# Optimization experiments

Hardware: AMD Instinct MI355X
Metric: run time of the kernel (lower is better)

Reference implementation:

```python
import jax, jax.numpy as jnp
import numpy as np

N_HEADS = 16

def setup_inputs() -> dict:
    key = jax.random.key(0)
    k1, k2, k3 = jax.random.split(key, 3)
    d = 1024
    x = jax.random.normal(k1, (2, 2048, d), dtype=jnp.float32)
    W_in = jax.random.normal(k2, (d, 3 * d), dtype=jnp.float32) * (d ** -0.5)
    W_out = jax.random.normal(k3, (d, d), dtype=jnp.float32) * (d ** -0.5)
    return {"x": x, "W_in": W_in, "W_out": W_out}

def reference(x, W_in, W_out):
    B, S, D = x.shape
    H = N_HEADS
    Dh = D // H
    qkv = x @ W_in                                  # [B,S,3D]
    q, k, v = jnp.split(qkv, 3, axis=-1)
    # [B,S,D] -> [B,H,S,Dh]
    q = q.reshape(B, S, H, Dh).transpose(0, 2, 1, 3)
    k = k.reshape(B, S, H, Dh).transpose(0, 2, 1, 3)
    v = v.reshape(B, S, H, Dh).transpose(0, 2, 1, 3)
    scores = jnp.einsum('bhqd,bhkd->bhqk', q, k)    # [B,H,S,S]
    causal = jnp.triu(jnp.ones((S, S), dtype=bool), k=1)
    scores = jnp.where(causal, -jnp.inf, scores)
    scores = scores / jnp.sqrt(jnp.asarray(Dh, scores.dtype))
    attn = jax.nn.softmax(scores, axis=-1)
    out = jnp.einsum('bhqk,bhkd->bhqd', attn, v)    # [B,H,S,Dh]
    out = out.transpose(0, 2, 1, 3).reshape(B, S, D)
    return out @ W_out
```

## Files before the change

kernel.cpp:

```cpp
#include <hip/hip_runtime.h>
#include <cstdint>
#include <cstddef>

typedef __bf16 bf16;
typedef bf16  bf16x4  __attribute__((ext_vector_type(4)));
typedef bf16  bf16x8  __attribute__((ext_vector_type(8)));
typedef float floatx4 __attribute__((ext_vector_type(4)));

#define BATCH 2
#define SEQ   2048
#define DIM   1024
#define NH    16
#define DH    64
#define D3    3072
#define MROWS 4096

__device__ __forceinline__ void gld16(void* lds, const void* gptr) {
  __builtin_amdgcn_global_load_lds(
      (const __attribute__((address_space(1))) unsigned int*)gptr,
      (__attribute__((address_space(3))) unsigned int*)lds, 16, 0, 0);
}

__global__ __launch_bounds__(256) void k_convert_x(const float4* __restrict__ in,
                                                   bf16* __restrict__ out) {
  int i = blockIdx.x * 256 + threadIdx.x;
  float4 v = in[i];
  bf16x4 o;
  o.x = (bf16)v.x; o.y = (bf16)v.y; o.z = (bf16)v.z; o.w = (bf16)v.w;
  *(bf16x4*)(out + (size_t)i * 4) = o;
}

__global__ __launch_bounds__(256) void k_transpose_w(const float* __restrict__ W,
                                                     bf16* __restrict__ Wt,
                                                     int K, int N) {
  __shared__ float tile[32][33];
  int k0 = blockIdx.y * 32, n0 = blockIdx.x * 32;
  int tx = threadIdx.x & 31, ty = threadIdx.x >> 5;
#pragma unroll
  for (int i = 0; i < 4; i++)
    tile[ty + i * 8][tx] = W[(size_t)(k0 + ty + i * 8) * N + n0 + tx];
  __syncthreads();
#pragma unroll
  for (int i = 0; i < 4; i++)
    Wt[(size_t)(n0 + ty + i * 8) * K + k0 + tx] = (bf16)tile[tx][ty + i * 8];
}

template <typename OutT, int MODE>
__global__ __launch_bounds__(256) void k_gemm_bt(const bf16* __restrict__ A,
                                                 const bf16* __restrict__ Bt,
                                                 OutT* __restrict__ C,
                                                 bf16* __restrict__ qk,
                                                 bf16* __restrict__ vt,
                                                 int M, int N, int K) {
  __shared__ __align__(16) bf16 As[128 * 32];
  __shared__ __align__(16) bf16 Bs[128 * 32];
  const int t = threadIdx.x, l = t & 63, w = t >> 6;
  const int wr = w >> 1, wc = w & 1;
  const int q = l >> 4, mm = l & 15;
  const int m0 = blockIdx.y * 128, n0 = blockIdx.x * 128;
  const int sw = (mm >> 1) & 3;

  floatx4 acc[4][4] = {};

  for (int kt = 0; kt < K; kt += 32) {
    __syncthreads();
#pragma unroll
    for (int i = 0; i < 2; i++) {
      int c = t + i * 256;
      int row = c >> 2, pos = c & 3;
      int g = pos ^ ((row >> 1) & 3);
      gld16((char*)As + (size_t)c * 16, A  + (size_t)(m0 + row) * K + kt + g * 8);
      gld16((char*)Bs + (size_t)c * 16, Bt + (size_t)(n0 + row) * K + kt + g * 8);
    }
    __syncthreads();
    bf16x8 af[4], bfr[4];
#pragma unroll
    for (int mt = 0; mt < 4; mt++)
      af[mt] = *(const bf16x8*)(As + (size_t)(wr * 64 + mt * 16 + mm) * 32 + (q ^ sw) * 8);
#pragma unroll
    for (int nt = 0; nt < 4; nt++)
      bfr[nt] = *(const bf16x8*)(Bs + (size_t)(wc * 64 + nt * 16 + mm) * 32 + (q ^ sw) * 8);
#pragma unroll
    for (int mt = 0; mt < 4; mt++)
#pragma unroll
      for (int nt = 0; nt < 4; nt++)
        acc[mt][nt] = __builtin_amdgcn_mfma_f32_16x16x32_bf16(af[mt], bfr[nt],
                                                              acc[mt][nt], 0, 0, 0);
  }
#pragma unroll
  for (int mt = 0; mt < 4; mt++)
#pragma unroll
    for (int nt = 0; nt < 4; nt++)
#pragma unroll
      for (int r = 0; r < 4; r++) {
        int row = m0 + wr * 64 + mt * 16 + q * 4 + r;
        int col = n0 + wc * 64 + nt * 16 + mm;
        if (MODE == 0) {
          C[(size_t)row * N + col] = (OutT)acc[mt][nt][r];
        } else {
          if (n0 < 2048) {
            qk[(size_t)row * 2048 + col] = (bf16)acc[mt][nt][r];
          } else {
            int d = col - 2048;
            int hh = d >> 6, dh = d & 63;
            int bb = row >> 11, s = row & 2047;
            vt[((size_t)(bb * 16 + hh) * 64 + dh) * SEQ + s] = (bf16)acc[mt][nt][r];
          }
        }
      }
}

__global__ __launch_bounds__(256, 4) void k_attn(const bf16* __restrict__ qk,
                                                 const bf16* __restrict__ vt,
                                                 bf16* __restrict__ out) {
  const int bx = blockIdx.x;
  const int qt = 31 - (bx >> 5);
  const int bh = bx & 31;
  const int b = bh >> 4, h = bh & 15;
  const int t = threadIdx.x, l = t & 63, w = t >> 6;
  const int q4 = l >> 4, mm = l & 15;
  const int sw = (mm >> 1) & 3;

  __shared__ __align__(16) char lds[8192 + 16384 + 16384];
  bf16* Qs = (bf16*)lds;
  bf16* Ps = (bf16*)lds;
  bf16* Ks = (bf16*)(lds + 8192);
  bf16* Vs = (bf16*)(lds + 8192 + 16384);

  const size_t qkbase = (size_t)b * SEQ * 2048;
  const size_t vtbase = (size_t)bh * 64 * SEQ;

  auto stage = [&](int kt) {
    const int bp = kt & 1;
#pragma unroll
    for (int i = 0; i < 2; i++) {
      int row = t >> 2, pos = t & 3;
      int g = pos ^ ((row >> 1) & 3);
      gld16((char*)(Ks + bp * 4096) + ((size_t)t + i * 256) * 16,
            qk + qkbase + (size_t)(kt * 64 + row) * 2048 + 1024 + h * 64 + i * 32 + g * 8);
    }
#pragma unroll
    for (int i = 0; i < 2; i++) {
      int c = t + i * 256;
      int vr = c >> 3, vc = c & 7;
      int src = vc ^ (vr & 7);
      gld16((char*)(Vs + bp * 4096) + (size_t)c * 16,
            vt + vtbase + (size_t)vr * SEQ + kt * 64 + src * 8);
    }
  };

  {
    int row = t >> 2, col = (t & 3) * 8;
#pragma unroll
    for (int i = 0; i < 2; i++)
      gld16((char*)Qs + ((size_t)t + i * 256) * 16,
            qk + qkbase + (size_t)(qt * 64 + row) * 2048 + h * 64 + i * 32 + col);
  }
  stage(0);
  __syncthreads();
  bf16x8 qf[2];
#pragma unroll
  for (int ks = 0; ks < 2; ks++) {
    qf[ks] = *(const bf16x8*)(Qs + (size_t)(ks * 64 + w * 16 + mm) * 32 + q4 * 8);
#pragma unroll
    for (int j = 0; j < 8; j++)
      qf[ks][j] = (bf16)((float)qf[ks][j] * 0.18033688f);
  }
  __syncthreads();

  float l_i = 0.f;
  floatx4 oaccT[4] = {};
  const int qloc = w * 16 + mm;
  const float FM = 24.0f;

  bf16* Pw = Ps + (size_t)w * 640;

  for (int kt = 0; kt <= qt; kt++) {
    if (kt < qt) stage(kt + 1);
    const bf16* Kb = Ks + (kt & 1) * 4096;
    const bf16* Vb = Vs + (kt & 1) * 4096;

    floatx4 sacc[4] = {};
#pragma unroll
    for (int ks = 0; ks < 2; ks++)
#pragma unroll
      for (int ct = 0; ct < 4; ct++) {
        bf16x8 kf = *(const bf16x8*)(Kb + (size_t)(ks * 64 + ct * 16 + mm) * 32 + (q4 ^ sw) * 8);
        sacc[ct] = __builtin_amdgcn_mfma_f32_16x16x32_bf16(kf, qf[ks], sacc[ct], 0, 0, 0);
      }

    bf16x4 pk[4];
    float rsum = 0.f;
    if (kt == qt) {
#pragma unroll
      for (int ct = 0; ct < 4; ct++)
#pragma unroll
        for (int r = 0; r < 4; r++) {
          float e = (ct * 16 + q4 * 4 + r > qloc)
                        ? 0.f : __builtin_amdgcn_exp2f(sacc[ct][r] - FM);
          pk[ct][r] = (bf16)e;
          rsum += e;
        }
    } else {
#pragma unroll
      for (int ct = 0; ct < 4; ct++)
#pragma unroll
        for (int r = 0; r < 4; r++) {
          float e = __builtin_amdgcn_exp2f(sacc[ct][r] - FM);
          pk[ct][r] = (bf16)e;
          rsum += e;
        }
    }
    rsum += __shfl_xor(rsum, 16, 64);
    rsum += __shfl_xor(rsum, 32, 64);
    l_i += rsum;

#pragma unroll
    for (int ks = 0; ks < 2; ks++) {
      *(bf16x4*)(Pw + (size_t)mm * 40 + q4 * 4)      = pk[ks * 2 + 0];
      *(bf16x4*)(Pw + (size_t)mm * 40 + 16 + q4 * 4) = pk[ks * 2 + 1];
      bf16x8 pf = *(const bf16x8*)(Pw + (size_t)mm * 40 + q4 * 8);
#pragma unroll
      for (int nt = 0; nt < 4; nt++) {
        int chunk = (ks * 4 + q4) ^ (mm & 7);
        bf16x8 vf = *(const bf16x8*)(Vb + (size_t)(nt * 16 + mm) * 64 + chunk * 8);
        oaccT[nt] = __builtin_amdgcn_mfma_f32_16x16x32_bf16(vf, pf, oaccT[nt], 0, 0, 0);
      }
    }

    if (kt < qt) __syncthreads();
  }

  float inv = 1.0f / l_i;
  int qrow = qt * 64 + qloc;
  bf16* orow = out + ((size_t)b * SEQ + qrow) * DIM + h * 64;
#pragma unroll
  for (int nt = 0; nt < 4; nt++) {
    bf16x4 o4;
#pragma unroll
    for (int r = 0; r < 4; r++) o4[r] = (bf16)(oaccT[nt][r] * inv);
    *(bf16x4*)(orow + nt * 16 + q4 * 4) = o4;
  }
}

extern "C" void kernel_launch(void* const* d_in, const int* in_sizes, int n_in,
                              void* d_out, int out_size, void* d_ws, size_t ws_size,
                              hipStream_t stream) {
  const float* x     = (const float*)d_in[0];
  const float* W_in  = (const float*)d_in[1];
  const float* W_out = (const float*)d_in[2];
  float* out = (float*)d_out;

  char* ws = (char*)d_ws;
  bf16* xb   = (bf16*)(ws);
  bf16* wti  = (bf16*)(ws + 8388608);
  bf16* wto  = (bf16*)(ws + 14680064);
  bf16* qkb  = (bf16*)(ws + 16777216);
  bf16* vtb  = (bf16*)(ws + 33554432);
  bf16* attn = xb;

  k_convert_x<<<4096, 256, 0, stream>>>((const float4*)x, xb);
  k_transpose_w<<<dim3(96, 32), 256, 0, stream>>>(W_in, wti, 1024, 3072);
  k_transpose_w<<<dim3(32, 32), 256, 0, stream>>>(W_out, wto, 1024, 1024);
  k_gemm_bt<bf16, 1><<<dim3(24, 32), 256, 0, stream>>>(xb, wti, nullptr, qkb, vtb,
                                                       MROWS, D3, DIM);
  k_attn<<<1024, 256, 0, stream>>>(qkb, vtb, attn);
  k_gemm_bt<float, 0><<<dim3(8, 32), 256, 0, stream>>>(attn, wto, out, nullptr, nullptr,
                                                       MROWS, DIM, DIM);
}
```

Baseline: 187.5 us.

## Double-buffer GEMM LDS tiles and merge prep kernels into one launch

The GEMM now keeps two LDS buffers and issues the global-to-LDS loads for the next K tile before computing the current one, leaving one barrier per iteration instead of two. The goal is to overlap memory latency with MFMA work. The x conversion and both weight transposes are folded into a single kernel launch, cutting two launches. LDS use doubles, which could lower occupancy. The async gld16 loads also rely on the barrier to make the next buffer safe to read.

```diff
diff --git a/kernel.cpp b/kernel.cpp
--- a/kernel.cpp
+++ b/kernel.cpp
@@ -21,20 +21,27 @@
       (__attribute__((address_space(3))) unsigned int*)lds, 16, 0, 0);
 }
 
-__global__ __launch_bounds__(256) void k_convert_x(const float4* __restrict__ in,
-                                                   bf16* __restrict__ out) {
-  int i = blockIdx.x * 256 + threadIdx.x;
-  float4 v = in[i];
-  bf16x4 o;
-  o.x = (bf16)v.x; o.y = (bf16)v.y; o.z = (bf16)v.z; o.w = (bf16)v.w;
-  *(bf16x4*)(out + (size_t)i * 4) = o;
-}
-
-__global__ __launch_bounds__(256) void k_transpose_w(const float* __restrict__ W,
-                                                     bf16* __restrict__ Wt,
-                                                     int K, int N) {
+__global__ __launch_bounds__(256) void k_prep(const float4* __restrict__ x,
+                                              bf16* __restrict__ xb,
+                                              const float* __restrict__ Wi,
+                                              bf16* __restrict__ wti,
+                                              const float* __restrict__ Wo,
+                                              bf16* __restrict__ wto) {
   __shared__ float tile[32][33];
-  int k0 = blockIdx.y * 32, n0 = blockIdx.x * 32;
+  const int bid = blockIdx.x;
+  if (bid < 4096) {
+    int i = bid * 256 + threadIdx.x;
+    float4 v = x[i];
+    bf16x4 o;
+    o.x = (bf16)v.x; o.y = (bf16)v.y; o.z = (bf16)v.z; o.w = (bf16)v.w;
+    *(bf16x4*)(xb + (size_t)i * 4) = o;
+    return;
+  }
+  const float* W; bf16* Wt; int N, id;
+  if (bid < 7168) { W = Wi; Wt = wti; N = 3072; id = bid - 4096; }
+  else            { W = Wo; Wt = wto; N = 1024; id = bid - 7168; }
+  const int nb = N / 32;
+  int n0 = (id % nb) * 32, k0 = (id / nb) * 32;
   int tx = threadIdx.x & 31, ty = threadIdx.x >> 5;
 #pragma unroll
   for (int i = 0; i < 4; i++)
@@ -42,7 +49,7 @@
   __syncthreads();
 #pragma unroll
   for (int i = 0; i < 4; i++)
-    Wt[(size_t)(n0 + ty + i * 8) * K + k0 + tx] = (bf16)tile[tx][ty + i * 8];
+    Wt[(size_t)(n0 + ty + i * 8) * 1024 + k0 + tx] = (bf16)tile[tx][ty + i * 8];
 }
 
 template <typename OutT, int MODE>
@@ -52,40 +59,50 @@
                                                  bf16* __restrict__ qk,
                                                  bf16* __restrict__ vt,
                                                  int M, int N, int K) {
-  __shared__ __align__(16) bf16 As[128 * 32];
-  __shared__ __align__(16) bf16 Bs[128 * 32];
+  __shared__ __align__(16) bf16 As[2][128 * 32];
+  __shared__ __align__(16) bf16 Bs[2][128 * 32];
   const int t = threadIdx.x, l = t & 63, w = t >> 6;
   const int wr = w >> 1, wc = w & 1;
   const int q = l >> 4, mm = l & 15;
   const int m0 = blockIdx.y * 128, n0 = blockIdx.x * 128;
   const int sw = (mm >> 1) & 3;
 
-  floatx4 acc[4][4] = {};
-
-  for (int kt = 0; kt < K; kt += 32) {
-    __syncthreads();
+  auto stage = [&](int kt) {
+    const int bp = kt & 1;
 #pragma unroll
     for (int i = 0; i < 2; i++) {
       int c = t + i * 256;
       int row = c >> 2, pos = c & 3;
       int g = pos ^ ((row >> 1) & 3);
-      gld16((char*)As + (size_t)c * 16, A  + (size_t)(m0 + row) * K + kt + g * 8);
-      gld16((char*)Bs + (size_t)c * 16, Bt + (size_t)(n0 + row) * K + kt + g * 8);
-    }
-    __syncthreads();
+      gld16((char*)As[bp] + (size_t)c * 16, A  + (size_t)(m0 + row) * K + kt * 32 + g * 8);
+      gld16((char*)Bs[bp] + (size_t)c * 16, Bt + (size_t)(n0 + row) * K + kt * 32 + g * 8);
+    }
+  };
+
+  floatx4 acc[4][4] = {};
+  const int nk = K >> 5;
+
+  stage(0);
+  __syncthreads();
+
+  for (int kt = 0; kt < nk; kt++) {
+    if (kt + 1 < nk) stage(kt + 1);
+    const bf16* Ab = As[kt & 1];
+    const bf16* Bb = Bs[kt & 1];
     bf16x8 af[4], bfr[4];
 #pragma unroll
     for (int mt = 0; mt < 4; mt++)
-      af[mt] = *(const bf16x8*)(As + (size_t)(wr * 64 + mt * 16 + mm) * 32 + (q ^ sw) * 8);
+      af[mt] = *(const bf16x8*)(Ab + (size_t)(wr * 64 + mt * 16 + mm) * 32 + (q ^ sw) * 8);
 #pragma unroll
     for (int nt = 0; nt < 4; nt++)
-      bfr[nt] = *(const bf16x8*)(Bs + (size_t)(wc * 64 + nt * 16 + mm) * 32 + (q ^ sw) * 8);
+      bfr[nt] = *(const bf16x8*)(Bb + (size_t)(wc * 64 + nt * 16 + mm) * 32 + (q ^ sw) * 8);
 #pragma unroll
     for (int mt = 0; mt < 4; mt++)
 #pragma unroll
       for (int nt = 0; nt < 4; nt++)
         acc[mt][nt] = __builtin_amdgcn_mfma_f32_16x16x32_bf16(af[mt], bfr[nt],
                                                               acc[mt][nt], 0, 0, 0);
+    if (kt + 1 < nk) __syncthreads();
   }
 #pragma unroll
   for (int mt = 0; mt < 4; mt++)
@@ -259,9 +276,7 @@
   bf16* vtb  = (bf16*)(ws + 33554432);
   bf16* attn = xb;
 
-  k_convert_x<<<4096, 256, 0, stream>>>((const float4*)x, xb);
-  k_transpose_w<<<dim3(96, 32), 256, 0, stream>>>(W_in, wti, 1024, 3072);
-  k_transpose_w<<<dim3(32, 32), 256, 0, stream>>>(W_out, wto, 1024, 1024);
+  k_prep<<<8192, 256, 0, stream>>>((const float4*)x, xb, W_in, wti, W_out, wto);
   k_gemm_bt<bf16, 1><<<dim3(24, 32), 256, 0, stream>>>(xb, wti, nullptr, qkb, vtb,
                                                        MROWS, D3, DIM);
   k_attn<<<1024, 256, 0, stream>>>(qkb, vtb, attn);
```

Measured after the change: 180.8 us. 1.04x faster.
